# Performance work log

Measured on AMD Instinct MI355X. Metric: run time of the kernel, lower is better.

The kernel has to match this reference:

```python
import jax, jax.numpy as jnp
import numpy as np

NUM_HEADS = 8


def setup_inputs() -> dict:
    key = jax.random.key(0)
    ks = jax.random.split(key, 5)
    b, c, h, w = 8, 256, 32, 32
    x = jax.random.normal(ks[0], (b, c, h, w), dtype=jnp.float32)
    w_qkv = jax.random.normal(ks[1], (3 * c, c), dtype=jnp.float32) * (c ** -0.5)
    b_qkv = jax.random.normal(ks[2], (3 * c,), dtype=jnp.float32) * 0.02
    w_proj = jax.random.normal(ks[3], (c, c), dtype=jnp.float32) * (c ** -0.5)
    b_proj = jax.random.normal(ks[4], (c,), dtype=jnp.float32) * 0.02
    return {"x": x, "w_qkv": w_qkv, "b_qkv": b_qkv, "w_proj": w_proj, "b_proj": b_proj}


def reference(x, w_qkv, b_qkv, w_proj, b_proj):
    b, c, h, w = x.shape
    nh = NUM_HEADS
    dh = c // nh
    L = h * w
    scale = dh ** -0.5
    # 1x1 conv == per-pixel GEMM
    qkv = jnp.einsum('bchw,oc->bohw', x, w_qkv) + b_qkv[None, :, None, None]
    qkv = qkv.reshape(b, 3, nh, dh, L)
    q, k, v = qkv[:, 0], qkv[:, 1], qkv[:, 2]  # each (b, nh, dh, L)
    attn = jnp.einsum('bhdi,bhdj->bhij', q, k) * scale  # (b, nh, L, L)
    attn = jax.nn.softmax(attn, axis=-1)
    out = jnp.einsum('bhdj,bhij->bhdi', v, attn)  # (b, nh, dh, L)
    out = out.reshape(b, c, h, w)
    proj = jnp.einsum('bchw,oc->bohw', out, w_proj) + b_proj[None, :, None, None]
    return x + proj
```

## Files before the change

### kernel.cpp

```cpp
#include <hip/hip_runtime.h>
#include <math.h>

#define B_   8
#define CIN  256
#define L_   1024
#define NH_  8
#define DH_  32

typedef __attribute__((ext_vector_type(8))) short short8;
typedef __attribute__((ext_vector_type(4))) short short4v;
typedef __attribute__((ext_vector_type(4))) float f32x4;
typedef __attribute__((ext_vector_type(4))) unsigned int uint4v;
typedef __attribute__((ext_vector_type(2))) unsigned int uint2v;

__device__ inline short f2bf_hu(float f) {
    union { float f; unsigned u; } v; v.f = f;
    return (short)((v.u + 0x8000u) >> 16);
}
__device__ inline float bf2f(short s) {
    union { unsigned u; float f; } v; v.u = ((unsigned)(unsigned short)s) << 16;
    return v.f;
}
__device__ inline unsigned pkbf2(float a, float b) {
    union { float f; unsigned u; } x, y; x.f = a; y.f = b;
    return __builtin_amdgcn_perm(y.u + 0x8000u, x.u + 0x8000u, 0x07060302u);
}
__device__ inline void glds16(const void* g, void* l) {
    __builtin_amdgcn_global_load_lds(
        (const __attribute__((address_space(1))) void*)g,
        (__attribute__((address_space(3))) void*)l, 16, 0, 0);
}

__global__ __launch_bounds__(256) void wconv(
    const float* __restrict__ wq, const float* __restrict__ wp,
    short* __restrict__ w2)
{
    const size_t e = ((size_t)blockIdx.x * 256 + threadIdx.x) * 8;
    const float* src = (e < (size_t)768 * 256) ? wq + e : wp + (e - (size_t)768 * 256);
    const float4 a = *(const float4*)src;
    const float4 c = *(const float4*)(src + 4);
    uint4v pk = { pkbf2(a.x, a.y), pkbf2(a.z, a.w),
                  pkbf2(c.x, c.y), pkbf2(c.z, c.w) };
    *(uint4v*)(w2 + e) = pk;
}

__global__ __launch_bounds__(256) void qkv_gemm(
    const float* __restrict__ x, const short* __restrict__ w2,
    const float* __restrict__ bias, short* __restrict__ qkv3)
{
    __shared__ __align__(16) short Xs[2][64][40];
    __shared__ __align__(16) short Wt[2][128][32];
    const int t = threadIdx.x, lane = t & 63, wv = t >> 6;
    const int n = lane & 15, quad = lane >> 4;
    const int b = blockIdx.z, o0 = blockIdx.y * 128, l0 = blockIdx.x * 64;

    float bias_r[8];
    #pragma unroll
    for (int nf = 0; nf < 8; nf++) bias_r[nf] = bias[o0 + nf * 16 + n];

    f32x4 acc[8];
    #pragma unroll
    for (int nf = 0; nf < 8; nf++) acc[nf] = (f32x4){0.f, 0.f, 0.f, 0.f};

    const int cS = t >> 3, lsS = (t & 7) * 8;

    const int oA = wv * 32 + (lane >> 2);
    const int cc = (lane & 3) ^ ((oA >> 1) & 3);
    const short* wpA = w2 + (size_t)(o0 + oA) * 256 + cc * 8;
    const short* wpB = wpA + 16 * 256;
    short* const ldsW0 = &Wt[0][0][0] + wv * 1024;
    short* const ldsW1 = &Wt[1][0][0] + wv * 1024;

    auto xwrite = [&](int buf, const float4& a, const float4& c) {
        const float vals[8] = {a.x, a.y, a.z, a.w, c.x, c.y, c.z, c.w};
        #pragma unroll
        for (int k = 0; k < 8; k++) {
            const int ll = lsS + k;
            const int col = (((cS >> 3) ^ (ll & 3)) << 3) | (cS & 7);
            Xs[buf][ll][col] = f2bf_hu(vals[k]);
        }
    };

    const float* xp = &x[(((size_t)b * CIN + cS) << 10) + l0 + lsS];
    float4 xa = *(const float4*)xp, xb = *(const float4*)(xp + 4);
    glds16(wpA, ldsW0);
    glds16(wpB, ldsW0 + 512);
    xwrite(0, xa, xb);
    xp += (size_t)32 << 10;
    xa = *(const float4*)xp; xb = *(const float4*)(xp + 4);

    const int wsw = (quad ^ ((n >> 1) & 3)) * 8;
    const int arow = wv * 16 + n;
    const int xsw = (quad ^ (arow & 3)) * 8;

    #pragma unroll
    for (int it = 0; it < 8; it++) {
        const int cur = it & 1;
        __syncthreads();
        if (it < 7) {
            short* ldsn = (cur ? ldsW0 : ldsW1);
            glds16(wpA + (it + 1) * 32, ldsn);
            glds16(wpB + (it + 1) * 32, ldsn + 512);
        }
        const short8 af = *(const short8*)&Xs[cur][arow][xsw];
        #pragma unroll
        for (int nf = 0; nf < 8; nf++) {
            const short8 bf = *(const short8*)&Wt[cur][nf * 16 + n][wsw];
            acc[nf] = __builtin_amdgcn_mfma_f32_16x16x32_bf16(af, bf, acc[nf], 0, 0, 0);
        }
        if (it < 7) {
            xwrite(cur ^ 1, xa, xb);
            if (it < 6) {
                xp += (size_t)32 << 10;
                xa = *(const float4*)xp; xb = *(const float4*)(xp + 4);
            }
        }
    }

    #pragma unroll
    for (int reg = 0; reg < 4; reg++) {
        const size_t l = l0 + wv * 16 + quad * 4 + reg;
        #pragma unroll
        for (int nf = 0; nf < 8; nf++) {
            const int o = o0 + nf * 16;
            const int tpl = o >> 8, hh = (o >> 5) & 7, dh0 = o & 31;
            short* dst = qkv3 + (((size_t)(tpl * 64 + b * 8 + hh)) << 15)
                              + l * 32 + dh0 + n;
            *dst = f2bf_hu(acc[nf][reg] + bias_r[nf]);
        }
    }
}

__global__ __launch_bounds__(256) void proj_gemm(
    const short* __restrict__ partO, const float* __restrict__ partD,
    const short* __restrict__ w2, const float* __restrict__ bias,
    const float* __restrict__ resid, float* __restrict__ out)
{
    __shared__ __align__(16) short Xs[2][64][40];
    __shared__ __align__(16) short Wt[2][64][32];
    const int t = threadIdx.x, lane = t & 63, wv = t >> 6;
    const int n = lane & 15, quad = lane >> 4;
    const int b = blockIdx.z, o0 = blockIdx.y * 64, l0 = blockIdx.x * 64;

    float bias_r[4];
    #pragma unroll
    for (int reg = 0; reg < 4; reg++) bias_r[reg] = bias[o0 + wv * 16 + quad * 4 + reg];

    f32x4 acc[4];
    #pragma unroll
    for (int nf = 0; nf < 4; nf++) acc[nf] = (f32x4){0.f, 0.f, 0.f, 0.f};

    const int l = t >> 2, cs = (t & 3) * 8;
    const size_t li = ((size_t)b << 10) + l0 + l;
    const short* p0 = &partO[(0 * (size_t)B_ * L_ + li) * CIN + cs];
    const short* p1 = &partO[(1 * (size_t)B_ * L_ + li) * CIN + cs];
    const float* pd0 = &partD[(0 * (size_t)B_ * L_ + li) * NH_];
    const float* pd1 = &partD[(1 * (size_t)B_ * L_ + li) * NH_];

    const int og = wv * 16 + (lane >> 2);
    const int ccg = (lane & 3) ^ ((og >> 1) & 3);
    const short* wp = w2 + (size_t)(o0 + og) * 256 + ccg * 8;
    short* const ldsW0 = &Wt[0][0][0] + wv * 512;
    short* const ldsW1 = &Wt[1][0][0] + wv * 512;

    short8 s0, s1;
    float d0, d1;
    auto combine_write = [&](int buf) {
        const float inv = 1.f / (d0 + d1);
        float v[8];
        #pragma unroll
        for (int e = 0; e < 8; e++) v[e] = (bf2f(s0[e]) + bf2f(s1[e])) * inv;
        uint4v pw = { pkbf2(v[0], v[1]), pkbf2(v[2], v[3]),
                      pkbf2(v[4], v[5]), pkbf2(v[6], v[7]) };
        *(uint4v*)&Xs[buf][l][cs] = pw;
    };

    s0 = *(const short8*)p0; s1 = *(const short8*)p1;
    d0 = pd0[0]; d1 = pd1[0];
    glds16(wp, ldsW0);
    combine_write(0);
    p0 += 32; p1 += 32;
    s0 = *(const short8*)p0; s1 = *(const short8*)p1;
    d0 = pd0[1]; d1 = pd1[1];

    const int wsw = (quad ^ ((n >> 1) & 3)) * 8;
    #pragma unroll
    for (int it = 0; it < 8; it++) {
        const int cur = it & 1;
        __syncthreads();
        if (it < 7) glds16(wp + (it + 1) * 32, cur ? ldsW0 : ldsW1);
        const short8 af = *(const short8*)&Wt[cur][wv * 16 + n][wsw];
        #pragma unroll
        for (int nf = 0; nf < 4; nf++) {
            const short8 bf = *(const short8*)&Xs[cur][nf * 16 + n][quad * 8];
            acc[nf] = __builtin_amdgcn_mfma_f32_16x16x32_bf16(af, bf, acc[nf], 0, 0, 0);
        }
        if (it < 7) {
            combine_write(cur ^ 1);
            if (it < 6) {
                p0 += 32; p1 += 32;
                s0 = *(const short8*)p0; s1 = *(const short8*)p1;
                d0 = pd0[it + 2]; d1 = pd1[it + 2];
            }
        }
    }

    #pragma unroll
    for (int reg = 0; reg < 4; reg++) {
        const int o = o0 + wv * 16 + quad * 4 + reg;
        #pragma unroll
        for (int nf = 0; nf < 4; nf++) {
            const size_t off = (((size_t)b * CIN + o) << 10) + l0 + nf * 16 + n;
            out[off] = acc[nf][reg] + bias_r[reg] + resid[off];
        }
    }
}

__global__ __launch_bounds__(256) void attn_mfma(
    const short* __restrict__ qkv3, short* __restrict__ partO,
    float* __restrict__ partD)
{
    __shared__ short Vt[2][32][80];
    __shared__ __align__(16) short Ss[128][88];

    const int t = threadIdx.x, lane = t & 63, wv = t >> 6;
    const int n = lane & 15, quad = lane >> 4;
    const int id = blockIdx.x;
    const int bh = id & 63;
    const int b = bh >> 3, h = bh & 7;
    const int i0 = ((id >> 6) & 7) * 128;
    const int s  = id >> 9;

    const short* qbase = qkv3 + ((size_t)(b * 8 + h) << 15);
    const short* kbase = qbase + ((size_t)64 << 15);
    const short* vbase = qbase + ((size_t)128 << 15);

    short8 qa[2];
    #pragma unroll
    for (int a = 0; a < 2; a++)
        qa[a] = *(const short8*)&qbase[(size_t)(i0 + wv * 32 + a * 16 + n) * 32
                                       + quad * 8];

    short8 vf2;
    {
        const short one = (n == 0) ? (short)0x3F80 : (short)0;
        #pragma unroll
        for (int u = 0; u < 8; u++) vf2[u] = one;
    }

    f32x4 o_acc[2][3];
    #pragma unroll
    for (int a = 0; a < 2; a++)
        #pragma unroll
        for (int nf = 0; nf < 3; nf++) o_acc[a][nf] = (f32x4){0.f, 0.f, 0.f, 0.f};

    const float K1 = 0.25503510f;
    const float K2 = 11.54156036f;
    const int TSTRIDE = 64 * 32;

    const size_t soff = (size_t)s * 8 * TSTRIDE;
    const short* kp0 = kbase + soff + (size_t)n * 32 + quad * 8;
    const short* kp1 = kp0 + 16 * 32;
    const short* kp2 = kp0 + 32 * 32;
    const short* kp3 = kp0 + 48 * 32;
    const int jS = t >> 3, dsS = (t & 7) * 4;
    const short* vp0 = vbase + soff + (size_t)jS * 32 + dsS;
    const short* vp1 = vp0 + 32 * 32;

    const int vmsk = ((dsS >> 2) & 7) << 3;
    const int vwo0 = dsS * 80 + (jS ^ vmsk);
    const int vwo1 = dsS * 80 + ((jS + 32) ^ vmsk);
    short* const vtb0 = &Vt[0][0][0];
    short* const vtb1 = &Vt[1][0][0];
    short* const ssw  = &Ss[wv * 32 + n][quad * 4];
    const short* const ssr = &Ss[wv * 32 + n][quad * 8];
    int vro[2][2];
    #pragma unroll
    for (int nf = 0; nf < 2; nf++) {
        const int dv = nf * 16 + n;
        const int msk = ((dv >> 2) & 7) << 3;
        #pragma unroll
        for (int kk = 0; kk < 2; kk++)
            vro[kk][nf] = dv * 80 + ((kk * 32 + quad * 8) ^ msk);
    }

    short8 kfA[4], kfB[4];

    auto stageV = [&](short* vtb) {
        const short4v a = *(const short4v*)vp0; vp0 += TSTRIDE;
        const short4v c = *(const short4v*)vp1; vp1 += TSTRIDE;
        #pragma unroll
        for (int u = 0; u < 4; u++) {
            vtb[vwo0 + u * 80] = a[u];
            vtb[vwo1 + u * 80] = c[u];
        }
    };
    auto loadK = [&](short8* kf) {
        kf[0] = *(const short8*)kp0; kp0 += TSTRIDE;
        kf[1] = *(const short8*)kp1; kp1 += TSTRIDE;
        kf[2] = *(const short8*)kp2; kp2 += TSTRIDE;
        kf[3] = *(const short8*)kp3; kp3 += TSTRIDE;
    };
    auto tile = [&](const short8* kf, const short* vtb) {
        #pragma unroll
        for (int f = 0; f < 4; f++) {
            #pragma unroll
            for (int a = 0; a < 2; a++) {
                f32x4 z = {0.f, 0.f, 0.f, 0.f};
                const f32x4 sv = __builtin_amdgcn_mfma_f32_16x16x32_bf16(kf[f], qa[a], z, 0, 0, 0);
                const float p0 = __builtin_amdgcn_exp2f(fmaf(sv[0], K1, -K2));
                const float p1 = __builtin_amdgcn_exp2f(fmaf(sv[1], K1, -K2));
                const float p2 = __builtin_amdgcn_exp2f(fmaf(sv[2], K1, -K2));
                const float p3 = __builtin_amdgcn_exp2f(fmaf(sv[3], K1, -K2));
                uint2v pk = { pkbf2(p0, p1), pkbf2(p2, p3) };
                *(uint2v*)(ssw + a * 16 * 88 + f * 16) = pk;
            }
        }
        #pragma unroll
        for (int kk = 0; kk < 2; kk++) {
            short8 pf[2];
            #pragma unroll
            for (int a = 0; a < 2; a++)
                pf[a] = *(const short8*)(ssr + a * 16 * 88 + kk * 32);
            #pragma unroll
            for (int nf = 0; nf < 2; nf++) {
                const short8 vf = *(const short8*)(vtb + vro[kk][nf]);
                #pragma unroll
                for (int a = 0; a < 2; a++)
                    o_acc[a][nf] = __builtin_amdgcn_mfma_f32_16x16x32_bf16(pf[a], vf, o_acc[a][nf], 0, 0, 0);
            }
            #pragma unroll
            for (int a = 0; a < 2; a++)
                o_acc[a][2] = __builtin_amdgcn_mfma_f32_16x16x32_bf16(pf[a], vf2, o_acc[a][2], 0, 0, 0);
        }
    };

    stageV(vtb0);
    loadK(kfA);

    for (int itp = 0; itp < 4; itp++) {
        __syncthreads();
        stageV(vtb1);
        loadK(kfB);
        tile(kfA, vtb0);
        __syncthreads();
        if (itp < 3) { stageV(vtb0); loadK(kfA); }
        tile(kfB, vtb1);
    }

    #pragma unroll
    for (int a = 0; a < 2; a++) {
        #pragma unroll
        for (int r = 0; r < 4; r++) {
            const int il = i0 + wv * 32 + a * 16 + quad * 4 + r;
            short* po = partO + (((size_t)s * B_ + b) * L_ + il) * CIN + h * DH_;
            po[n]      = f2bf_hu(o_acc[a][0][r]);
            po[16 + n] = f2bf_hu(o_acc[a][1][r]);
        }
    }
    if (n == 0) {
        #pragma unroll
        for (int a = 0; a < 2; a++)
            #pragma unroll
            for (int r = 0; r < 4; r++) {
                const int il = i0 + wv * 32 + a * 16 + quad * 4 + r;
                partD[(((size_t)s * B_ + b) * L_ + il) * NH_ + h] = o_acc[a][2][r];
            }
    }
}

extern "C" void kernel_launch(void* const* d_in, const int* in_sizes, int n_in,
                              void* d_out, int out_size, void* d_ws, size_t ws_size,
                              hipStream_t stream) {
    const float* x      = (const float*)d_in[0];
    const float* w_qkv  = (const float*)d_in[1];
    const float* b_qkv  = (const float*)d_in[2];
    const float* w_proj = (const float*)d_in[3];
    const float* b_proj = (const float*)d_in[4];
    float* out = (float*)d_out;

    short* qkv3  = (short*)d_ws;
    short* partO = qkv3 + (size_t)B_ * L_ * 768;
    float* partD = (float*)(partO + (size_t)2 * B_ * L_ * CIN);
    short* w2    = (short*)(partD + (size_t)2 * B_ * L_ * NH_);

    wconv<<<dim3(128), 256, 0, stream>>>(w_qkv, w_proj, w2);
    qkv_gemm<<<dim3(16, 6, B_), 256, 0, stream>>>(x, w2, b_qkv, qkv3);
    attn_mfma<<<dim3(1024), 256, 0, stream>>>(qkv3, partO, partD);
    proj_gemm<<<dim3(16, 4, B_), 256, 0, stream>>>(partO, partD, w2 + (size_t)768 * 256,
                                                   b_proj, x, out);
}
```

Measured before the change: 109.7 us.

## Keep attention probabilities in registers using 32x32 MFMA, drop LDS P round-trip

Rewrites the attention inner tile to use 32x32x16 bf16 MFMAs and computes S transposed, so each lane's P values already sit in the A-operand layout for the PV MFMA. This removes the shared-memory staging of P and its extra LDS writes and reads. The softmax denominator is now a per-lane register sum plus a cross-half shuffle, replacing the extra ones-vector MFMA. The cost is a changed V fragment read pattern (two 8-byte LDS reads per operand) and more accumulator registers.

```diff
diff --git a/kernel.cpp b/kernel.cpp
--- a/kernel.cpp
+++ b/kernel.cpp
@@ -10,8 +10,8 @@
 typedef __attribute__((ext_vector_type(8))) short short8;
 typedef __attribute__((ext_vector_type(4))) short short4v;
 typedef __attribute__((ext_vector_type(4))) float f32x4;
+typedef __attribute__((ext_vector_type(16))) float f32x16;
 typedef __attribute__((ext_vector_type(4))) unsigned int uint4v;
-typedef __attribute__((ext_vector_type(2))) unsigned int uint2v;
 
 __device__ inline short f2bf_hu(float f) {
     union { float f; unsigned u; } v; v.f = f;
@@ -221,10 +221,9 @@
     float* __restrict__ partD)
 {
     __shared__ short Vt[2][32][80];
-    __shared__ __align__(16) short Ss[128][88];
 
     const int t = threadIdx.x, lane = t & 63, wv = t >> 6;
-    const int n = lane & 15, quad = lane >> 4;
+    const int il = lane & 31, h2 = lane >> 5;
     const int id = blockIdx.x;
     const int bh = id & 63;
     const int b = bh >> 3, h = bh & 7;
@@ -235,34 +234,21 @@
     const short* kbase = qbase + ((size_t)64 << 15);
     const short* vbase = qbase + ((size_t)128 << 15);
 
-    short8 qa[2];
-    #pragma unroll
-    for (int a = 0; a < 2; a++)
-        qa[a] = *(const short8*)&qbase[(size_t)(i0 + wv * 32 + a * 16 + n) * 32
-                                       + quad * 8];
-
-    short8 vf2;
-    {
-        const short one = (n == 0) ? (short)0x3F80 : (short)0;
-        #pragma unroll
-        for (int u = 0; u < 8; u++) vf2[u] = one;
-    }
-
-    f32x4 o_acc[2][3];
-    #pragma unroll
-    for (int a = 0; a < 2; a++)
-        #pragma unroll
-        for (int nf = 0; nf < 3; nf++) o_acc[a][nf] = (f32x4){0.f, 0.f, 0.f, 0.f};
+    const short* qp = qbase + (size_t)(i0 + wv * 32 + il) * 32 + h2 * 8;
+    const short8 qa0 = *(const short8*)qp;
+    const short8 qa1 = *(const short8*)(qp + 16);
+
+    f32x16 o_acc = {0.f,0.f,0.f,0.f,0.f,0.f,0.f,0.f,
+                    0.f,0.f,0.f,0.f,0.f,0.f,0.f,0.f};
+    float dsum = 0.f;
 
     const float K1 = 0.25503510f;
     const float K2 = 11.54156036f;
     const int TSTRIDE = 64 * 32;
-
     const size_t soff = (size_t)s * 8 * TSTRIDE;
-    const short* kp0 = kbase + soff + (size_t)n * 32 + quad * 8;
-    const short* kp1 = kp0 + 16 * 32;
-    const short* kp2 = kp0 + 32 * 32;
-    const short* kp3 = kp0 + 48 * 32;
+
+    const short* kp = kbase + soff + (size_t)il * 32 + h2 * 8;
+
     const int jS = t >> 3, dsS = (t & 7) * 4;
     const short* vp0 = vbase + soff + (size_t)jS * 32 + dsS;
     const short* vp1 = vp0 + 32 * 32;
@@ -272,17 +258,14 @@
     const int vwo1 = dsS * 80 + ((jS + 32) ^ vmsk);
     short* const vtb0 = &Vt[0][0][0];
     short* const vtb1 = &Vt[1][0][0];
-    short* const ssw  = &Ss[wv * 32 + n][quad * 4];
-    const short* const ssr = &Ss[wv * 32 + n][quad * 8];
-    int vro[2][2];
-    #pragma unroll
-    for (int nf = 0; nf < 2; nf++) {
-        const int dv = nf * 16 + n;
-        const int msk = ((dv >> 2) & 7) << 3;
-        #pragma unroll
-        for (int kk = 0; kk < 2; kk++)
-            vro[kk][nf] = dv * 80 + ((kk * 32 + quad * 8) ^ msk);
-    }
+
+    const int rmsk = ((il >> 2) & 7) << 3;
+    int vro2[2][4];
+    #pragma unroll
+    for (int js = 0; js < 2; js++)
+        #pragma unroll
+        for (int g = 0; g < 4; g++)
+            vro2[js][g] = il * 80 + ((js * 32 + g * 8 + 4 * h2) ^ rmsk);
 
     short8 kfA[4], kfB[4];
 
@@ -296,42 +279,37 @@
         }
     };
     auto loadK = [&](short8* kf) {
-        kf[0] = *(const short8*)kp0; kp0 += TSTRIDE;
-        kf[1] = *(const short8*)kp1; kp1 += TSTRIDE;
-        kf[2] = *(const short8*)kp2; kp2 += TSTRIDE;
-        kf[3] = *(const short8*)kp3; kp3 += TSTRIDE;
+        kf[0] = *(const short8*)kp;
+        kf[1] = *(const short8*)(kp + 16);
+        kf[2] = *(const short8*)(kp + 1024);
+        kf[3] = *(const short8*)(kp + 1024 + 16);
+        kp += TSTRIDE;
     };
     auto tile = [&](const short8* kf, const short* vtb) {
         #pragma unroll
-        for (int f = 0; f < 4; f++) {
+        for (int js = 0; js < 2; js++) {
+            const f32x16 Z = {0.f,0.f,0.f,0.f,0.f,0.f,0.f,0.f,
+                              0.f,0.f,0.f,0.f,0.f,0.f,0.f,0.f};
+            f32x16 sv = __builtin_amdgcn_mfma_f32_32x32x16_bf16(kf[js*2],   qa0, Z,  0, 0, 0);
+            sv        = __builtin_amdgcn_mfma_f32_32x32x16_bf16(kf[js*2+1], qa1, sv, 0, 0, 0);
+            unsigned c[8];
             #pragma unroll
-            for (int a = 0; a < 2; a++) {
-                f32x4 z = {0.f, 0.f, 0.f, 0.f};
-                const f32x4 sv = __builtin_amdgcn_mfma_f32_16x16x32_bf16(kf[f], qa[a], z, 0, 0, 0);
-                const float p0 = __builtin_amdgcn_exp2f(fmaf(sv[0], K1, -K2));
-                const float p1 = __builtin_amdgcn_exp2f(fmaf(sv[1], K1, -K2));
-                const float p2 = __builtin_amdgcn_exp2f(fmaf(sv[2], K1, -K2));
-                const float p3 = __builtin_amdgcn_exp2f(fmaf(sv[3], K1, -K2));
-                uint2v pk = { pkbf2(p0, p1), pkbf2(p2, p3) };
-                *(uint2v*)(ssw + a * 16 * 88 + f * 16) = pk;
+            for (int pi = 0; pi < 8; pi++) {
+                const float pl = __builtin_amdgcn_exp2f(fmaf(sv[2*pi],   K1, -K2));
+                const float ph = __builtin_amdgcn_exp2f(fmaf(sv[2*pi+1], K1, -K2));
+                dsum += pl; dsum += ph;
+                c[pi] = pkbf2(pl, ph);
             }
-        }
-        #pragma unroll
-        for (int kk = 0; kk < 2; kk++) {
-            short8 pf[2];
-            #pragma unroll
-            for (int a = 0; a < 2; a++)
-                pf[a] = *(const short8*)(ssr + a * 16 * 88 + kk * 32);
-            #pragma unroll
-            for (int nf = 0; nf < 2; nf++) {
-                const short8 vf = *(const short8*)(vtb + vro[kk][nf]);
-                #pragma unroll
-                for (int a = 0; a < 2; a++)
-                    o_acc[a][nf] = __builtin_amdgcn_mfma_f32_16x16x32_bf16(pf[a], vf, o_acc[a][nf], 0, 0, 0);
-            }
-            #pragma unroll
-            for (int a = 0; a < 2; a++)
-                o_acc[a][2] = __builtin_amdgcn_mfma_f32_16x16x32_bf16(pf[a], vf2, o_acc[a][2], 0, 0, 0);
+            union { unsigned u[4]; short8 s8; } pa0, pa1;
+            pa0.u[0] = c[0]; pa0.u[1] = c[1]; pa0.u[2] = c[2]; pa0.u[3] = c[3];
+            pa1.u[0] = c[4]; pa1.u[1] = c[5]; pa1.u[2] = c[6]; pa1.u[3] = c[7];
+            union { short4v h4[2]; short8 s8; } vf0, vf1;
+            vf0.h4[0] = *(const short4v*)(vtb + vro2[js][0]);
+            vf0.h4[1] = *(const short4v*)(vtb + vro2[js][1]);
+            o_acc = __builtin_amdgcn_mfma_f32_32x32x16_bf16(pa0.s8, vf0.s8, o_acc, 0, 0, 0);
+            vf1.h4[0] = *(const short4v*)(vtb + vro2[js][2]);
+            vf1.h4[1] = *(const short4v*)(vtb + vro2[js][3]);
+            o_acc = __builtin_amdgcn_mfma_f32_32x32x16_bf16(pa1.s8, vf1.s8, o_acc, 0, 0, 0);
         }
     };
 
@@ -348,25 +326,16 @@
         tile(kfB, vtb1);
     }
 
-    #pragma unroll
-    for (int a = 0; a < 2; a++) {
-        #pragma unroll
-        for (int r = 0; r < 4; r++) {
-            const int il = i0 + wv * 32 + a * 16 + quad * 4 + r;
-            short* po = partO + (((size_t)s * B_ + b) * L_ + il) * CIN + h * DH_;
-            po[n]      = f2bf_hu(o_acc[a][0][r]);
-            po[16 + n] = f2bf_hu(o_acc[a][1][r]);
-        }
-    }
-    if (n == 0) {
-        #pragma unroll
-        for (int a = 0; a < 2; a++)
-            #pragma unroll
-            for (int r = 0; r < 4; r++) {
-                const int il = i0 + wv * 32 + a * 16 + quad * 4 + r;
-                partD[(((size_t)s * B_ + b) * L_ + il) * NH_ + h] = o_acc[a][2][r];
-            }
-    }
+    const float dtot = dsum + __shfl_xor(dsum, 32);
+    #pragma unroll
+    for (int r = 0; r < 16; r++) {
+        const int irow = (r & 3) + 8 * (r >> 2) + 4 * h2;
+        const int ig = i0 + wv * 32 + irow;
+        partO[(((size_t)s * B_ + b) * L_ + ig) * CIN + h * DH_ + il]
+            = f2bf_hu(o_acc[r]);
+    }
+    if (lane < 32)
+        partD[(((size_t)s * B_ + b) * L_ + (i0 + wv * 32 + il)) * NH_ + h] = dtot;
 }
 
 extern "C" void kernel_launch(void* const* d_in, const int* in_sizes, int n_in,
```

New measurement: 107.7 us. No clear change (-1.8%).
